# Performance work log

Measured on AMD Instinct MI355X. Metric: run time of the kernel, lower is better.

The kernel has to match this reference:

```python
import jax, jax.numpy as jnp
import numpy as np

B, D, FH, FW, C = 8, 41, 32, 88, 64
OGFH, OGFW = 512, 1408
DX = jnp.array([0.5, 20.0, 0.5], dtype=jnp.float32)          # voxel sizes (x, y, z)
BX = jnp.array([-49.75, 0.0, -49.75], dtype=jnp.float32)    # voxel centers origin
NX = (200, 1, 200)                                           # grid dims (x, y, z)
NSEG = NX[0] * NX[1] * NX[2] * B                             # 320000 voxel-batch slots


def _frustum():
    # (D, FH, FW, 3) pixel-u, pixel-v, depth; matches create_frustum_1camera
    ds = jnp.broadcast_to(jnp.arange(4.0, 45.0, 1.0)[:, None, None], (D, FH, FW))
    xs = jnp.broadcast_to(jnp.linspace(0.0, OGFW - 1, FW)[None, None, :], (D, FH, FW))
    ys = jnp.broadcast_to(jnp.linspace(0.0, OGFH - 1, FH)[None, :, None], (D, FH, FW))
    return jnp.stack([xs, ys, ds], axis=-1).astype(jnp.float32)


def setup_inputs() -> dict:
    key = jax.random.key(0)
    k1, = jax.random.split(key, 1)
    x = jax.random.normal(k1, (B, D, FH, FW, C), dtype=jnp.float32)
    # realistic pinhole intrinsics: fx=fy=800, principal point at image center
    K = np.array([[800.0, 0.0, OGFW / 2.0],
                  [0.0, 800.0, OGFH / 2.0],
                  [0.0, 0.0, 1.0]], dtype=np.float32)
    intrins = jnp.asarray(np.broadcast_to(K, (B, 3, 3)).copy())
    post_rots = jnp.broadcast_to(jnp.eye(3, dtype=jnp.float32), (B, 3, 3)) + jnp.zeros((B, 3, 3), jnp.float32)
    post_trans = jnp.zeros((B, 3), dtype=jnp.float32)
    return {"x": x, "intrins": intrins, "post_rots": post_rots, "post_trans": post_trans}


def _forward(x, intrins, post_rots, post_trans):
    # ---- get_geometry ----
    pts = _frustum()[None] - post_trans[:, None, None, None, :]          # (B,D,FH,FW,3)
    pts = jnp.einsum('bij,bdhwj->bdhwi', jnp.linalg.inv(post_rots), pts)
    pts = jnp.concatenate([pts[..., :2] * pts[..., 2:3], pts[..., 2:3]], axis=-1)
    geom = jnp.einsum('bij,bdhwj->bdhwi', jnp.linalg.inv(intrins), pts)  # camera-frame xyz

    # ---- voxel_splat ----
    Nprime = B * D * FH * FW
    xf = x.reshape(Nprime, C)
    # torch .long() truncates toward zero -> float->int cast in jnp also truncates
    coords = ((geom - (BX - DX / 2.0)) / DX).reshape(Nprime, 3).astype(jnp.int32)
    batch_ix = jnp.repeat(jnp.arange(B, dtype=jnp.int32), Nprime // B)
    kept = ((coords[:, 0] >= 0) & (coords[:, 0] < NX[0]) &
            (coords[:, 1] >= 0) & (coords[:, 1] < NX[1]) &
            (coords[:, 2] >= 0) & (coords[:, 2] < NX[2]))
    ranks = (coords[:, 0] * (NX[1] * NX[2] * B) + coords[:, 1] * (NX[2] * B) +
             coords[:, 2] * B + batch_ix)
    ranks = jnp.where(kept, ranks, NSEG)  # dump out-of-grid points into extra segment
    # segment-sum == sort + cumsum-trick pooling (sum of features per voxel)
    pooled = jax.ops.segment_sum(xf, ranks, num_segments=NSEG + 1)[:-1]  # (NSEG, C)
    final = pooled.reshape(NX[0], NX[1], NX[2], B, C)       # rank order: (x, y, z, b)
    final = jnp.transpose(final, (3, 4, 1, 2, 0))            # (B, C, ny, nz, nx)
    # torch.cat(final.unbind(dim=2), 1) -> stack ny slices along channel dim
    out = jnp.transpose(final, (0, 2, 1, 3, 4)).reshape(B, NX[1] * C, NX[2], NX[0])
    return out


def reference(x, intrins, post_rots, post_trans):
    return _forward(x, intrins, post_rots, post_trans)
```

## Files before the change

### kernel.cpp

```cpp
#include <hip/hip_runtime.h>

#define BB 8
#define DD 41
#define FHH 32
#define FWW 88
#define CC 64
#define NXX 200
#define NXZ 200
#define PLANE (NXZ * NXX)
#define NBD (BB * DD)
#define NHALF (2 * NBD)
#define NROWS (BB * NXZ)
#define NWG 11
#define PAD 204
#define STEPX (1407.0f / 87.0f)
#define STEPY (511.0f / 31.0f)

#define MM_OFF 0
#define CX_OFF (NBD * FWW)
#define CZ_OFF (2 * NBD * FWW)
#define CS_OFF (CZ_OFF + NBD)

__device__ __forceinline__ float invEntry(const float* __restrict__ a, int e) {
#pragma clang fp contract(off)
    float c00 = a[4] * a[8] - a[5] * a[7];
    float c01 = a[5] * a[6] - a[3] * a[8];
    float c02 = a[3] * a[7] - a[4] * a[6];
    float det = a[0] * c00 + a[1] * c01 + a[2] * c02;
    float num;
    switch (e) {
        case 0: num = c00; break;
        case 1: num = a[2] * a[7] - a[1] * a[8]; break;
        case 2: num = a[1] * a[5] - a[2] * a[4]; break;
        case 3: num = c01; break;
        case 4: num = a[0] * a[8] - a[2] * a[6]; break;
        case 5: num = a[2] * a[3] - a[0] * a[5]; break;
        case 6: num = c02; break;
        case 7: num = a[1] * a[6] - a[0] * a[7]; break;
        default: num = a[0] * a[4] - a[1] * a[3]; break;
    }
    return num / det;
}

__device__ __forceinline__ int cz_of(const float* iR, const float* iK,
                                     float t0, float t1, float t2, int d) {
#pragma clang fp contract(off)
    float dv = 4.0f + (float)d;
    float q0 = 0.0f - t0, q1 = 0.0f - t1, q2 = dv - t2;
    float p0 = fmaf(iR[2], q2, fmaf(iR[1], q1, iR[0] * q0));
    float p1 = fmaf(iR[5], q2, fmaf(iR[4], q1, iR[3] * q0));
    float p2 = fmaf(iR[8], q2, fmaf(iR[7], q1, iR[6] * q0));
    float s0 = p0 * p2, s1 = p1 * p2, s2 = p2;
    float g2 = fmaf(iK[8], s2, fmaf(iK[7], s1, iK[6] * s0));
    float czf = (g2 + 50.0f) * 2.0f;
    return (int)czf;
}

__global__ __launch_bounds__(256) void lss_meta(
        const float* __restrict__ intrins, const float* __restrict__ post_rots,
        const float* __restrict__ post_trans, int* __restrict__ wsI) {
#pragma clang fp contract(off)
    __shared__ float sInv[18];
    __shared__ unsigned smask[FWW];
    __shared__ int scx[FWW];
    __shared__ int smin, smax;
    int bd = blockIdx.x;
    int d = bd % DD, b = bd / DD;
    int tid = threadIdx.x;
    if (tid < 18) {
        const float* a = (tid < 9 ? post_rots : intrins) + b * 9;
        sInv[tid] = invEntry(a, tid % 9);
    }
    if (tid == 0) { smin = 1 << 30; smax = -1; }
    __syncthreads();
    const float* iR = sInv;
    const float* iK = sInv + 9;
    float t0 = post_trans[b * 3 + 0];
    float t1 = post_trans[b * 3 + 1];
    float t2 = post_trans[b * 3 + 2];
    float dv = 4.0f + (float)d;

    for (int t = tid; t < FWW * FHH; t += 256) {
        int w = t >> 5;
        int h = t & 31;
        float u = (float)w * STEPX;
        float v = (float)h * STEPY;
        float q0 = u - t0, q1 = v - t1, q2 = dv - t2;
        float p0 = fmaf(iR[2], q2, fmaf(iR[1], q1, iR[0] * q0));
        float p1 = fmaf(iR[5], q2, fmaf(iR[4], q1, iR[3] * q0));
        float p2 = fmaf(iR[8], q2, fmaf(iR[7], q1, iR[6] * q0));
        float s0 = p0 * p2, s1 = p1 * p2, s2 = p2;
        float g0 = fmaf(iK[2], s2, fmaf(iK[1], s1, iK[0] * s0));
        float g1 = fmaf(iK[5], s2, fmaf(iK[4], s1, iK[3] * s0));
        float g2 = fmaf(iK[8], s2, fmaf(iK[7], s1, iK[6] * s0));
        float cxf = (g0 + 50.0f) * 2.0f;
        float cyf = (g1 + 10.0f) / 20.0f;
        float czf = (g2 + 50.0f) * 2.0f;
        int cx = (int)cxf;
        int cy = (int)cyf;
        int cz = (int)czf;
        bool kept = (cx >= 0) & (cx < NXX) & (cy == 0) & (cz >= 0) & (cz < NXZ);
        unsigned long long m = __ballot(kept);
        int lane = tid & 63;
        int cxc = min(NXX - 1, max(0, cx));
        if (lane == 0) {
            smask[w] = (unsigned)m;          scx[w] = cxc;
            ((unsigned*)wsI)[MM_OFF + bd * FWW + w] = (unsigned)m;
            wsI[CX_OFF + bd * FWW + w] = cxc;
        } else if (lane == 32) {
            smask[w] = (unsigned)(m >> 32);  scx[w] = cxc;
            ((unsigned*)wsI)[MM_OFF + bd * FWW + w] = (unsigned)(m >> 32);
            wsI[CX_OFF + bd * FWW + w] = cxc;
        }
    }
    __syncthreads();
    if (tid < FWW && smask[tid]) {
        atomicMin(&smin, scx[tid]);
        atomicMax(&smax, scx[tid]);
    }
    __syncthreads();
    if (tid == 0) {
        wsI[CZ_OFF + bd] = cz_of(iR, iK, t0, t1, t2, d);
        wsI[CS_OFF + bd] = (smax < 0) ? 0 : ((smin + smax + 1) >> 1);
    }
}

__global__ __launch_bounds__(512) void lss_main(
        const float* __restrict__ x, const int* __restrict__ wsI,
        const float* __restrict__ intrins, const float* __restrict__ post_rots,
        const float* __restrict__ post_trans, float* __restrict__ out) {
#pragma clang fp contract(off)
    __shared__ float srow[CC * PAD];
    __shared__ unsigned sm[FWW];
    __shared__ int scx[FWW];
    __shared__ int sflag;
    int blk = blockIdx.x;
    int tid = threadIdx.x;

    if (blk >= NHALF) {
        int r = blk - NHALF;
        int b = r / NXZ, czr = r - b * NXZ;
        float* sInv = srow;
        if (tid < 18) {
            const float* a = (tid < 9 ? post_rots : intrins) + b * 9;
            sInv[tid] = invEntry(a, tid % 9);
        }
        __syncthreads();
        if (tid < 64) {
            bool cov = false;
            if (tid < DD)
                cov = (cz_of(sInv, sInv + 9, post_trans[b * 3], post_trans[b * 3 + 1],
                             post_trans[b * 3 + 2], tid) == czr);
            unsigned long long m = __ballot(cov);
            if (tid == 0) sflag = (m != 0ull);
        }
        __syncthreads();
        if (sflag) return;
        float4 z = make_float4(0.f, 0.f, 0.f, 0.f);
        size_t base = ((size_t)b * CC) * PLANE + (size_t)czr * NXX;
        for (int i = tid; i < CC * (NXX / 4); i += 512) {
            int c = i / (NXX / 4), q = i - c * (NXX / 4);
            *reinterpret_cast<float4*>(out + base + (size_t)c * PLANE + q * 4) = z;
        }
        return;
    }

    int bd = blk >> 1;
    int half = blk & 1;
    int b = bd / DD;
    int cz = wsI[CZ_OFF + bd];
    if (cz < 0 || cz >= NXZ) return;
    int cxs = wsI[CS_OFF + bd];
    int lo = half ? cxs : 0;
    int hi = half ? NXX : cxs;
    if (lo >= hi) return;

    if (tid < FWW) {
        sm[tid]  = ((const unsigned*)wsI)[MM_OFF + bd * FWW + tid];
        scx[tid] = wsI[CX_OFF + bd * FWW + tid];
    }
    for (int i = tid; i < CC * PAD; i += 512) srow[i] = 0.0f;
    __syncthreads();

    int wv = tid >> 6, lane = tid & 63;
    int cq = lane & 15, hsub = lane >> 4;

    for (int k = 0; k < NWG; ++k) {
        int w = wv + (k << 3);
        unsigned m = sm[w];
        int cx = scx[w];
        if (!m || cx < lo || cx >= hi) continue;
        const float* colp = x + ((size_t)bd * FHH * FWW + w) * CC + (cq << 2);
        float4 vals[8];
#pragma unroll
        for (int hh = 0; hh < 8; ++hh)
            vals[hh] = *reinterpret_cast<const float4*>(
                colp + (size_t)((hh << 2) + hsub) * (FWW * CC));
        float4 acc = make_float4(0.f, 0.f, 0.f, 0.f);
#pragma unroll
        for (int hh = 0; hh < 8; ++hh) {
            bool bt = (m >> ((hh << 2) + hsub)) & 1u;
            acc.x += bt ? vals[hh].x : 0.0f;
            acc.y += bt ? vals[hh].y : 0.0f;
            acc.z += bt ? vals[hh].z : 0.0f;
            acc.w += bt ? vals[hh].w : 0.0f;
        }
#pragma unroll
        for (int mm = 16; mm <= 32; mm <<= 1) {
            acc.x += __shfl_xor(acc.x, mm, 64);
            acc.y += __shfl_xor(acc.y, mm, 64);
            acc.z += __shfl_xor(acc.z, mm, 64);
            acc.w += __shfl_xor(acc.w, mm, 64);
        }
        if (hsub == 0) {
            atomicAdd(&srow[(cq * 4 + 0) * PAD + cx], acc.x);
            atomicAdd(&srow[(cq * 4 + 1) * PAD + cx], acc.y);
            atomicAdd(&srow[(cq * 4 + 2) * PAD + cx], acc.z);
            atomicAdd(&srow[(cq * 4 + 3) * PAD + cx], acc.w);
        }
    }
    __syncthreads();

    int n = hi - lo;
    size_t base = ((size_t)b * CC) * PLANE + (size_t)cz * NXX;
    for (int j = tid; j < CC * n; j += 512) {
        int ch = j / n;
        int cell = lo + (j - ch * n);
        out[base + (size_t)ch * PLANE + cell] = srow[ch * PAD + cell];
    }
}

extern "C" void kernel_launch(void* const* d_in, const int* in_sizes, int n_in,
                              void* d_out, int out_size, void* d_ws, size_t ws_size,
                              hipStream_t stream) {
    const float* x          = (const float*)d_in[0];
    const float* intrins    = (const float*)d_in[1];
    const float* post_rots  = (const float*)d_in[2];
    const float* post_trans = (const float*)d_in[3];
    float* out = (float*)d_out;
    int*   wsI = (int*)d_ws;

    lss_meta<<<NBD, 256, 0, stream>>>(intrins, post_rots, post_trans, wsI);
    lss_main<<<NHALF + NROWS, 512, 0, stream>>>(x, wsI, intrins, post_rots,
                                                post_trans, out);
}
```

Baseline: 76.81 us.

## Replace LDS atomic scatter with per-column sums and prefix-indexed segmented reduction

Each (batch,depth) row is now handled by a single block that sums masked heights per image column into shared memory without atomics. The meta kernel precomputes, for every voxel x index, how many columns map below it, so the writeback reduces contiguous column ranges and stores float4 outputs. This removes the two-half split, the shared atomics and the large zeroed buffer. The trade-offs are half as many blocks, no skipping of fully masked columns, and reliance on the column-to-cx mapping being monotone.

```diff
diff --git a/kernel.cpp b/kernel.cpp
--- a/kernel.cpp
+++ b/kernel.cpp
@@ -9,17 +9,13 @@
 #define NXZ 200
 #define PLANE (NXZ * NXX)
 #define NBD (BB * DD)
-#define NHALF (2 * NBD)
 #define NROWS (BB * NXZ)
-#define NWG 11
-#define PAD 204
 #define STEPX (1407.0f / 87.0f)
 #define STEPY (511.0f / 31.0f)
 
 #define MM_OFF 0
-#define CX_OFF (NBD * FWW)
-#define CZ_OFF (2 * NBD * FWW)
-#define CS_OFF (CZ_OFF + NBD)
+#define CZ_OFF (NBD * FWW)
+#define SLO_OFF (CZ_OFF + NBD)
 
 __device__ __forceinline__ float invEntry(const float* __restrict__ a, int e) {
 #pragma clang fp contract(off)
@@ -63,7 +59,6 @@
     __shared__ float sInv[18];
     __shared__ unsigned smask[FWW];
     __shared__ int scx[FWW];
-    __shared__ int smin, smax;
     int bd = blockIdx.x;
     int d = bd % DD, b = bd / DD;
     int tid = threadIdx.x;
@@ -71,7 +66,6 @@
         const float* a = (tid < 9 ? post_rots : intrins) + b * 9;
         sInv[tid] = invEntry(a, tid % 9);
     }
-    if (tid == 0) { smin = 1 << 30; smax = -1; }
     __syncthreads();
     const float* iR = sInv;
     const float* iK = sInv + 9;
@@ -104,25 +98,23 @@
         int lane = tid & 63;
         int cxc = min(NXX - 1, max(0, cx));
         if (lane == 0) {
-            smask[w] = (unsigned)m;          scx[w] = cxc;
+            smask[w] = (unsigned)m;
+            scx[w]   = cxc;
             ((unsigned*)wsI)[MM_OFF + bd * FWW + w] = (unsigned)m;
-            wsI[CX_OFF + bd * FWW + w] = cxc;
         } else if (lane == 32) {
-            smask[w] = (unsigned)(m >> 32);  scx[w] = cxc;
+            smask[w] = (unsigned)(m >> 32);
+            scx[w]   = cxc;
             ((unsigned*)wsI)[MM_OFF + bd * FWW + w] = (unsigned)(m >> 32);
-            wsI[CX_OFF + bd * FWW + w] = cxc;
-        }
-    }
-    __syncthreads();
-    if (tid < FWW && smask[tid]) {
-        atomicMin(&smin, scx[tid]);
-        atomicMax(&smax, scx[tid]);
-    }
-    __syncthreads();
-    if (tid == 0) {
+        }
+    }
+    __syncthreads();
+    for (int t = tid; t <= NXX; t += 256) {
+        int cnt = 0;
+        for (int w = 0; w < FWW; ++w) cnt += (scx[w] < t) ? 1 : 0;
+        wsI[SLO_OFF + bd * (NXX + 1) + t] = cnt;
+    }
+    if (tid == 0)
         wsI[CZ_OFF + bd] = cz_of(iR, iK, t0, t1, t2, d);
-        wsI[CS_OFF + bd] = (smax < 0) ? 0 : ((smin + smax + 1) >> 1);
-    }
 }
 
 __global__ __launch_bounds__(512) void lss_main(
@@ -130,17 +122,17 @@
         const float* __restrict__ intrins, const float* __restrict__ post_rots,
         const float* __restrict__ post_trans, float* __restrict__ out) {
 #pragma clang fp contract(off)
-    __shared__ float srow[CC * PAD];
-    __shared__ unsigned sm[FWW];
-    __shared__ int scx[FWW];
+    __shared__ float scol[FWW][CC + 1];
+    __shared__ int sslo[NXX + 1];
+    __shared__ unsigned ssm[FWW];
     __shared__ int sflag;
     int blk = blockIdx.x;
     int tid = threadIdx.x;
 
-    if (blk >= NHALF) {
-        int r = blk - NHALF;
+    if (blk >= NBD) {
+        int r = blk - NBD;
         int b = r / NXZ, czr = r - b * NXZ;
-        float* sInv = srow;
+        float* sInv = &scol[0][0];
         if (tid < 18) {
             const float* a = (tid < 9 ? post_rots : intrins) + b * 9;
             sInv[tid] = invEntry(a, tid % 9);
@@ -165,68 +157,54 @@
         return;
     }
 
-    int bd = blk >> 1;
-    int half = blk & 1;
+    int bd = blk;
     int b = bd / DD;
     int cz = wsI[CZ_OFF + bd];
     if (cz < 0 || cz >= NXZ) return;
-    int cxs = wsI[CS_OFF + bd];
-    int lo = half ? cxs : 0;
-    int hi = half ? NXX : cxs;
-    if (lo >= hi) return;
-
-    if (tid < FWW) {
-        sm[tid]  = ((const unsigned*)wsI)[MM_OFF + bd * FWW + tid];
-        scx[tid] = wsI[CX_OFF + bd * FWW + tid];
-    }
-    for (int i = tid; i < CC * PAD; i += 512) srow[i] = 0.0f;
+
+    if (tid < FWW) ssm[tid] = ((const unsigned*)wsI)[MM_OFF + bd * FWW + tid];
+    for (int t = tid; t <= NXX; t += 512) sslo[t] = wsI[SLO_OFF + bd * (NXX + 1) + t];
     __syncthreads();
 
     int wv = tid >> 6, lane = tid & 63;
-    int cq = lane & 15, hsub = lane >> 4;
-
-    for (int k = 0; k < NWG; ++k) {
-        int w = wv + (k << 3);
-        unsigned m = sm[w];
-        int cx = scx[w];
-        if (!m || cx < lo || cx >= hi) continue;
-        const float* colp = x + ((size_t)bd * FHH * FWW + w) * CC + (cq << 2);
-        float4 vals[8];
-#pragma unroll
-        for (int hh = 0; hh < 8; ++hh)
-            vals[hh] = *reinterpret_cast<const float4*>(
-                colp + (size_t)((hh << 2) + hsub) * (FWW * CC));
+    int wsub = lane >> 4, cq = lane & 15;
+
+    for (int g = wv; g < FWW / 4; g += 8) {
+        int w = g * 4 + wsub;
+        unsigned m = ssm[w];
+        const float* p = x + ((size_t)bd * FHH * FWW + w) * CC + (cq << 2);
         float4 acc = make_float4(0.f, 0.f, 0.f, 0.f);
-#pragma unroll
-        for (int hh = 0; hh < 8; ++hh) {
-            bool bt = (m >> ((hh << 2) + hsub)) & 1u;
-            acc.x += bt ? vals[hh].x : 0.0f;
-            acc.y += bt ? vals[hh].y : 0.0f;
-            acc.z += bt ? vals[hh].z : 0.0f;
-            acc.w += bt ? vals[hh].w : 0.0f;
-        }
-#pragma unroll
-        for (int mm = 16; mm <= 32; mm <<= 1) {
-            acc.x += __shfl_xor(acc.x, mm, 64);
-            acc.y += __shfl_xor(acc.y, mm, 64);
-            acc.z += __shfl_xor(acc.z, mm, 64);
-            acc.w += __shfl_xor(acc.w, mm, 64);
-        }
-        if (hsub == 0) {
-            atomicAdd(&srow[(cq * 4 + 0) * PAD + cx], acc.x);
-            atomicAdd(&srow[(cq * 4 + 1) * PAD + cx], acc.y);
-            atomicAdd(&srow[(cq * 4 + 2) * PAD + cx], acc.z);
-            atomicAdd(&srow[(cq * 4 + 3) * PAD + cx], acc.w);
-        }
-    }
-    __syncthreads();
-
-    int n = hi - lo;
+#pragma unroll 4
+        for (int h = 0; h < FHH; ++h) {
+            float4 v = *reinterpret_cast<const float4*>(p);
+            bool bt = (m >> h) & 1u;
+            acc.x += bt ? v.x : 0.0f;
+            acc.y += bt ? v.y : 0.0f;
+            acc.z += bt ? v.z : 0.0f;
+            acc.w += bt ? v.w : 0.0f;
+            p += FWW * CC;
+        }
+        scol[w][cq * 4 + 0] = acc.x;
+        scol[w][cq * 4 + 1] = acc.y;
+        scol[w][cq * 4 + 2] = acc.z;
+        scol[w][cq * 4 + 3] = acc.w;
+    }
+    __syncthreads();
+
     size_t base = ((size_t)b * CC) * PLANE + (size_t)cz * NXX;
-    for (int j = tid; j < CC * n; j += 512) {
-        int ch = j / n;
-        int cell = lo + (j - ch * n);
-        out[base + (size_t)ch * PLANE + cell] = srow[ch * PAD + cell];
+    for (int j = tid; j < CC * (NXX / 4); j += 512) {
+        int ch = j / (NXX / 4);
+        int qq = j - ch * (NXX / 4);
+        int c0 = qq * 4;
+        int e0 = sslo[c0], e1 = sslo[c0 + 1], e2 = sslo[c0 + 2],
+            e3 = sslo[c0 + 3], e4 = sslo[c0 + 4];
+        float4 o;
+        float s;
+        s = 0.f; for (int w = e0; w < e1; ++w) s += scol[w][ch]; o.x = s;
+        s = 0.f; for (int w = e1; w < e2; ++w) s += scol[w][ch]; o.y = s;
+        s = 0.f; for (int w = e2; w < e3; ++w) s += scol[w][ch]; o.z = s;
+        s = 0.f; for (int w = e3; w < e4; ++w) s += scol[w][ch]; o.w = s;
+        *reinterpret_cast<float4*>(out + base + (size_t)ch * PLANE + c0) = o;
     }
 }
 
@@ -241,6 +219,6 @@
     int*   wsI = (int*)d_ws;
 
     lss_meta<<<NBD, 256, 0, stream>>>(intrins, post_rots, post_trans, wsI);
-    lss_main<<<NHALF + NROWS, 512, 0, stream>>>(x, wsI, intrins, post_rots,
-                                                post_trans, out);
-}
+    lss_main<<<NBD + NROWS, 512, 0, stream>>>(x, wsI, intrins, post_rots,
+                                              post_trans, out);
+}
```

Result: slower. 79.10 us (+3.0%).
